# Optimization experiments

Hardware: AMD Instinct MI355X
Metric: run time of the kernel (lower is better)

Reference implementation:

```python
import jax, jax.numpy as jnp
import numpy as np

DECAY = 0.99
EPS = 1e-5
K = 512  # num_embeddings


def setup_inputs() -> dict:
    key = jax.random.key(0)
    k1, k2, k3 = jax.random.split(key, 3)
    B, C, H, W = 32, 64, 64, 64
    x = jax.random.normal(k1, (B, C, H, W), dtype=jnp.float32)
    codebook = jax.random.uniform(k2, (K, C), dtype=jnp.float32)
    ema_cluster_size = jnp.ones((K,), dtype=jnp.float32)
    ema_weight = jax.random.uniform(k3, (K, C), dtype=jnp.float32)
    return {"x": x, "codebook": codebook,
            "ema_cluster_size": ema_cluster_size, "ema_weight": ema_weight}


def reference(x, codebook, ema_cluster_size, ema_weight):
    B, C, H, W = x.shape
    # (B, C, H, W) -> (B*H*W, C)
    x_flat = jnp.transpose(x, (0, 2, 3, 1)).reshape(-1, C)

    x_sq = jnp.sum(x_flat * x_flat, axis=1, keepdims=True)        # [N, 1]
    e_sq = jnp.sum(codebook * codebook, axis=1)[None, :]          # [1, K]
    distances = x_sq + e_sq - 2.0 * (x_flat @ codebook.T)         # [N, K]
    indices = jnp.argmin(distances, axis=1)                        # [N]

    quantized = codebook[indices].reshape(B, H, W, C)
    quantized = jnp.transpose(quantized, (0, 3, 1, 2))             # [B, C, H, W]

    # EMA codebook update (training path); one-hot matmuls expressed as segment sums
    counts = jax.ops.segment_sum(jnp.ones_like(indices, dtype=x.dtype), indices,
                                 num_segments=K)                   # [K]
    sums = jax.ops.segment_sum(x_flat, indices, num_segments=K)    # [K, C]
    new_cluster_size = DECAY * ema_cluster_size + (1.0 - DECAY) * counts
    new_ema_weight = DECAY * ema_weight + (1.0 - DECAY) * sums
    n = jnp.sum(new_cluster_size)
    smoothed = (new_cluster_size + EPS) / (n + K * EPS) * n
    new_codebook = new_ema_weight / smoothed[:, None]

    commitment_loss = jnp.mean((x - jax.lax.stop_gradient(quantized)) ** 2)
    unique_codes = jnp.sum(counts > 0).astype(jnp.float32)

    out = x + jax.lax.stop_gradient(quantized - x)  # straight-through estimator
    return out, commitment_loss, unique_codes, new_codebook
```

## Files before the change

### kernel.cpp

```cpp
#include <hip/hip_runtime.h>


typedef __attribute__((ext_vector_type(8))) short bf16x8;
typedef __attribute__((ext_vector_type(16))) float f32x16;

#define MFMA32 __builtin_amdgcn_mfma_f32_32x32x16_bf16
#define NSEG 256

__device__ __forceinline__ unsigned short f2bf(float f) {
    unsigned u = __float_as_uint(f);
    return (unsigned short)((u + 0x7fffu + ((u >> 16) & 1u)) >> 16);
}
__device__ __forceinline__ float bf2f(unsigned short h) {
    return __uint_as_float(((unsigned)h) << 16);
}

__global__ void __launch_bounds__(512)
vq_prep(const float* __restrict__ cb, float* __restrict__ esq, char* __restrict__ cbF) {
    __shared__ float tile[64 * 65];
    const int tid = threadIdx.x;
    const int k0  = blockIdx.x * 64;
    #pragma unroll
    for (int i = tid; i < 4096; i += 512)
        tile[(i >> 6) * 65 + (i & 63)] = cb[k0 * 64 + i];
    __syncthreads();
    const int u  = tid >> 6;
    const int kl = tid & 63;
    const float* row = tile + kl * 65;
    const int cbase = (u >> 1) * 16 + (u & 1) * 8;
    bf16x8 h8, l8;
    #pragma unroll
    for (int j = 0; j < 8; ++j) {
        float e = row[cbase + j];
        unsigned short hb = f2bf(e);
        float lo = e - bf2f(hb);
        h8[j] = (short)hb;
        l8[j] = (short)f2bf(lo);
    }
    const size_t idx = (size_t)(u * 512 + k0 + kl) * 16;
    *(bf16x8*)(cbF + idx)         = h8;
    *(bf16x8*)(cbF + 65536 + idx) = l8;
    if (u == 0) {
        float s = 0.f;
        #pragma unroll
        for (int c = 0; c < 64; ++c) { float v = row[c]; s = fmaf(v, v, s); }
        esq[k0 + kl] = s;
    }
}

__device__ __forceinline__ void upd(float s, int kq, float& b1, int& q1, float& b2, int& q2) {
    bool t1 = s < b1;
    bool t2 = s < b2;
    float nb2 = t1 ? b1 : (t2 ? s : b2);
    int   nq2 = t1 ? q1 : (t2 ? kq : q2);
    b2 = nb2; q2 = nq2;
    b1 = t1 ? s : b1;
    q1 = t1 ? kq : q1;
}

__device__ __forceinline__ int refine_pair(int k1, int k2, long gx,
        const float* __restrict__ x, const float* __restrict__ cbg,
        const float* esq) {
    const float4* e1 = (const float4*)(cbg + (k1 << 6));
    const float4* e2 = (const float4*)(cbg + (k2 << 6));
    float a0 = 0.f, a1 = 0.f, c0 = 0.f, c1 = 0.f;
    #pragma unroll 4
    for (int j = 0; j < 16; ++j) {
        float4 ea = e1[j], eb = e2[j];
        float x0 = x[gx + (long)(4 * j + 0) * 4096];
        float x1 = x[gx + (long)(4 * j + 1) * 4096];
        float x2 = x[gx + (long)(4 * j + 2) * 4096];
        float x3 = x[gx + (long)(4 * j + 3) * 4096];
        a0 = fmaf(x0, ea.x, a0); a1 = fmaf(x1, ea.y, a1);
        a0 = fmaf(x2, ea.z, a0); a1 = fmaf(x3, ea.w, a1);
        c0 = fmaf(x0, eb.x, c0); c1 = fmaf(x1, eb.y, c1);
        c0 = fmaf(x2, eb.z, c0); c1 = fmaf(x3, eb.w, c1);
    }
    float s1 = esq[k1] - 2.f * (a0 + a1);
    float s2 = esq[k2] - 2.f * (c0 + c1);
    return (s2 < s1 || (s2 == s1 && k2 < k1)) ? k2 : k1;
}

#define AM_LDS_FLOATS 16896

__global__ void __launch_bounds__(512, 2)
vq_argmin(const float* __restrict__ x, const float* __restrict__ cbg,
          const float* __restrict__ esqg, const char* __restrict__ cbF,
          unsigned short* __restrict__ bkg, float* __restrict__ zero528) {
    extern __shared__ float lds[];
    float* esq = lds + 16384;
    const bf16x8* chi   = (const bf16x8*)lds;
    const bf16x8* clo_g = (const bf16x8*)(cbF + 65536);
    const int tid  = threadIdx.x;
    const int lane = tid & 63;
    const int wv   = tid >> 6;
    const int l31  = lane & 31;
    const int hh   = lane >> 5;

    {
        const float4* src = (const float4*)cbF;
        float4* dst = (float4*)lds;
        #pragma unroll
        for (int i = tid; i < 4096; i += 512) dst[i] = src[i];
        esq[tid] = esqg[tid];
    }
    zero528[tid] = 0.f;
    if (tid < 16) zero528[512 + tid] = 0.f;

    const int nb = blockIdx.x * 256 + wv * 32;
    bf16x8 Bh[4], Bl[4];
    {
        const int n = nb + l31;
        const long gx = (long)(n >> 12) * 262144 + (long)((n >> 6) & 63) * 64 + (n & 63);
        #pragma unroll
        for (int cs = 0; cs < 4; ++cs) {
            float v[8];
            #pragma unroll
            for (int j = 0; j < 8; ++j)
                v[j] = -2.f * x[gx + (long)(cs * 16 + hh * 8 + j) * 4096];
            union { unsigned u[4]; bf16x8 v8; } uh, ul;
            #pragma unroll
            for (int p = 0; p < 4; ++p) {
                unsigned hp, lp;
                asm("v_cvt_pk_bf16_f32 %0, %1, %2" : "=v"(hp) : "v"(v[2*p]), "v"(v[2*p+1]));
                float r0 = v[2*p]     - __uint_as_float(hp << 16);
                float r1 = v[2*p + 1] - __uint_as_float(hp & 0xFFFF0000u);
                asm("v_cvt_pk_bf16_f32 %0, %1, %2" : "=v"(lp) : "v"(r0), "v"(r1));
                uh.u[p] = hp; ul.u[p] = lp;
            }
            Bh[cs] = uh.v8; Bl[cs] = ul.v8;
        }
    }
    __syncthreads();

    float b1 = 3.4e38f, b2 = 3.4e38f;
    int   q1 = 0, q2 = 0;
    bf16x8 Xl[4], Yl[4];

#define LOADAL(Al, kt) { _Pragma("unroll") for (int cs = 0; cs < 4; ++cs) { \
        Al[cs] = clo_g[(cs * 2 + hh) * 512 + (kt) * 32 + l31]; } }

#define STEP(Al, kt) { \
        bf16x8 Ah[4]; \
        _Pragma("unroll") for (int cs = 0; cs < 4; ++cs) \
            Ah[cs] = chi[(cs * 2 + hh) * 512 + (kt) * 32 + l31]; \
        f32x16 acc; \
        _Pragma("unroll") for (int g = 0; g < 4; ++g) { \
            float4 e4 = *(const float4*)(esq + (kt) * 32 + 8 * g + 4 * hh); \
            acc[4*g] = e4.x; acc[4*g+1] = e4.y; acc[4*g+2] = e4.z; acc[4*g+3] = e4.w; } \
        _Pragma("unroll") for (int cs = 0; cs < 4; ++cs) { \
            acc = MFMA32(Ah[cs], Bh[cs], acc, 0, 0, 0); \
            acc = MFMA32(Al[cs], Bh[cs], acc, 0, 0, 0); \
            acc = MFMA32(Ah[cs], Bl[cs], acc, 0, 0, 0); } \
        _Pragma("unroll") for (int e = 0; e < 16; ++e) { \
            int kq = (kt) * 32 + (e & 3) + 8 * (e >> 2); \
            upd(acc[e], kq, b1, q1, b2, q2); } }

    LOADAL(Xl, 0)
    #pragma unroll 1
    for (int ktp = 0; ktp < 16; ktp += 2) {
        LOADAL(Yl, ktp + 1)
        STEP(Xl, ktp)
        if (ktp + 2 < 16) LOADAL(Xl, ktp + 2)
        STEP(Yl, ktp + 1)
    }

    {
        float mb1 = b1, mb2 = b2;
        int   mk1 = q1 + 4 * hh, mk2 = q2 + 4 * hh;
        float ob1 = __shfl_xor(mb1, 32, 64); int ok1 = __shfl_xor(mk1, 32, 64);
        float ob2 = __shfl_xor(mb2, 32, 64); int ok2 = __shfl_xor(mk2, 32, 64);
        bool t = (ob1 < mb1) || (ob1 == mb1 && ok1 < mk1);
        float w1 = t ? ob1 : mb1;  int wk1 = t ? ok1 : mk1;
        float l1 = t ? mb1 : ob1;  int lk1 = t ? mk1 : ok1;
        float w2c = t ? ob2 : mb2; int wk2c = t ? ok2 : mk2;
        bool t2 = (w2c < l1) || (w2c == l1 && wk2c < lk1);
        float w2 = t2 ? w2c : l1;  int wk2 = t2 ? wk2c : lk1;
        if (hh == 0) {
            int kk = wk1;
            if (wk2 != wk1 && (w2 - w1 < 2e-3f)) {
                const int n = nb + l31;
                const long gx = (long)(n >> 12) * 262144
                              + (long)((n >> 6) & 63) * 64 + (n & 63);
                kk = refine_pair(wk1, wk2, gx, x, cbg, esq);
            }
            bkg[nb + l31] = (unsigned short)kk;
        }
    }
#undef LOADAL
#undef STEP
}

#define FUSED_LDS_BYTES (33536 * 2)

__global__ void __launch_bounds__(512)
vq_fused(const float* __restrict__ x, const float* __restrict__ cbg,
         const unsigned short* __restrict__ bkg, float* __restrict__ out,
         float* __restrict__ hsum, float* __restrict__ acc_loss,
         float* __restrict__ slabs) {
    extern __shared__ unsigned short sm16[];
    const int tid = threadIdx.x;
    if (blockIdx.x < 256) {
        float* hist = (float*)sm16;
        float* lred = (float*)sm16 + 512;
        hist[tid] = 0.f;
        __syncthreads();
        const int n  = blockIdx.x * 512 + tid;
        const long gx = (long)(n >> 12) * 262144 + (long)((n >> 6) & 63) * 64 + (n & 63);
        const int k1 = bkg[n];
        atomicAdd(&hist[k1], 1.0f);
        const float4* q4 = (const float4*)(cbg + (k1 << 6));
        float lsum = 0.f;
        #pragma unroll
        for (int j = 0; j < 16; ++j) {
            float4 q = q4[j];
            const float qv[4] = {q.x, q.y, q.z, q.w};
            #pragma unroll
            for (int r = 0; r < 4; ++r) {
                const int c = 4 * j + r;
                float xc = x[gx + (long)c * 4096];
                out[gx + (long)c * 4096] = qv[r];
                float d = xc - qv[r];
                lsum = fmaf(d, d, lsum);
            }
        }
        #pragma unroll
        for (int o = 32; o > 0; o >>= 1) lsum += __shfl_down(lsum, o, 64);
        if ((tid & 63) == 0) lred[tid >> 6] = lsum;
        __syncthreads();
        if (tid == 0) {
            float l = ((lred[0] + lred[1]) + (lred[2] + lred[3]))
                    + ((lred[4] + lred[5]) + (lred[6] + lred[7]));
            atomicAdd(acc_loss, l);
        }
        { float v = hist[tid]; if (v != 0.f) atomicAdd(&hsum[tid], v); }
    } else {
        unsigned short* xb = sm16;
        unsigned short* kb = sm16 + 33024;
        const int lane = tid & 63;
        const int w    = tid >> 6;
        const int l31  = lane & 31;
        const int hh   = lane >> 5;
        const int bix  = blockIdx.x - 256;
        const int n0   = bix * 512;
        const float* xpl = x + (long)(n0 >> 12) * 262144 + (n0 & 4095);

        kb[tid] = bkg[n0 + tid];
        #pragma unroll
        for (int i = 0; i < 16; ++i) {
            const int f  = tid + i * 512;
            const int c  = f >> 7;
            const int n4 = (f & 127) << 2;
            float4 v = *(const float4*)(xpl + (long)c * 4096 + n4);
            ushort4 o;
            o.x = f2bf(v.x); o.y = f2bf(v.y); o.z = f2bf(v.z); o.w = f2bf(v.w);
            *(ushort4*)(xb + c * 516 + n4) = o;
        }
        __syncthreads();

        const int t0 = w * 32 + l31;
        const int t1 = (w + 8) * 32 + l31;
        f32x16 aA0 = {}, aA1 = {}, aB0 = {}, aB1 = {};

        #pragma unroll 1
        for (int b16 = 0; b16 < 32; ++b16) {
            const int nofs = b16 * 16 + hh * 8;
            ushort4 p0a = *(const ushort4*)(xb + l31 * 516 + nofs);
            ushort4 p0b = *(const ushort4*)(xb + l31 * 516 + nofs + 4);
            ushort4 p1a = *(const ushort4*)(xb + (32 + l31) * 516 + nofs);
            ushort4 p1b = *(const ushort4*)(xb + (32 + l31) * 516 + nofs + 4);
            bf16x8 Bf0, Bf1;
            Bf0[0] = (short)p0a.x; Bf0[1] = (short)p0a.y;
            Bf0[2] = (short)p0a.z; Bf0[3] = (short)p0a.w;
            Bf0[4] = (short)p0b.x; Bf0[5] = (short)p0b.y;
            Bf0[6] = (short)p0b.z; Bf0[7] = (short)p0b.w;
            Bf1[0] = (short)p1a.x; Bf1[1] = (short)p1a.y;
            Bf1[2] = (short)p1a.z; Bf1[3] = (short)p1a.w;
            Bf1[4] = (short)p1b.x; Bf1[5] = (short)p1b.y;
            Bf1[6] = (short)p1b.z; Bf1[7] = (short)p1b.w;
            ushort4 k4a = *(const ushort4*)(kb + nofs);
            ushort4 k4b = *(const ushort4*)(kb + nofs + 4);
            const int kk[8] = {k4a.x, k4a.y, k4a.z, k4a.w,
                               k4b.x, k4b.y, k4b.z, k4b.w};
            bf16x8 A0, A1;
            #pragma unroll
            for (int j = 0; j < 8; ++j) {
                A0[j] = (kk[j] == t0) ? (short)0x3F80 : (short)0;
                A1[j] = (kk[j] == t1) ? (short)0x3F80 : (short)0;
            }
            aA0 = MFMA32(A0, Bf0, aA0, 0, 0, 0);
            aA1 = MFMA32(A0, Bf1, aA1, 0, 0, 0);
            aB0 = MFMA32(A1, Bf0, aB0, 0, 0, 0);
            aB1 = MFMA32(A1, Bf1, aB1, 0, 0, 0);
        }
        float* slab = slabs + (long)bix * 32768;
        #pragma unroll
        for (int e = 0; e < 16; ++e) {
            const int row = (e & 3) + 8 * (e >> 2) + 4 * hh;
            slab[(w * 32 + row) * 64 + l31]            = aA0[e];
            slab[(w * 32 + row) * 64 + 32 + l31]       = aA1[e];
            slab[((w + 8) * 32 + row) * 64 + l31]      = aB0[e];
            slab[((w + 8) * 32 + row) * 64 + 32 + l31] = aB1[e];
        }
    }
}

__global__ void __launch_bounds__(512)
vq_final(const float* __restrict__ slabs, const float* __restrict__ hsum,
         const float* __restrict__ acc_loss, const float* __restrict__ ema_cs,
         const float* __restrict__ ema_w, float* __restrict__ out_scalars,
         float* __restrict__ out_cb) {
    __shared__ float sm[512];
    __shared__ float s_red[17];
    const int tid = threadIdx.x;
    float cnt = hsum[tid];
    float ncs = 0.99f * ema_cs[tid] + 0.01f * cnt;
    float v1 = ncs;
    float v2 = (cnt > 0.f) ? 1.f : 0.f;
    #pragma unroll
    for (int o = 32; o > 0; o >>= 1) {
        v1 += __shfl_down(v1, o, 64);
        v2 += __shfl_down(v2, o, 64);
    }
    const int wv = tid >> 6;
    if ((tid & 63) == 0) { s_red[wv] = v1; s_red[wv + 8] = v2; }
    __syncthreads();
    if (tid == 0) {
        float nn = 0.f, uq = 0.f;
        #pragma unroll
        for (int i = 0; i < 8; ++i) { nn += s_red[i]; uq += s_red[i + 8]; }
        s_red[16] = nn;
        if (blockIdx.x == 0) {
            out_scalars[0] = acc_loss[0] / 8388608.f;
            out_scalars[1] = uq;
        }
    }
    __syncthreads();
    float nn = s_red[16];
    sm[tid] = (ncs + 1e-5f) / (nn + 512.f * 1e-5f) * nn;
    __syncthreads();
    const int e = blockIdx.x * 512 + tid;
    float s = 0.f;
    #pragma unroll 8
    for (int b = 0; b < NSEG; ++b) s += slabs[(long)b * 32768 + e];
    float nw = 0.99f * ema_w[e] + 0.01f * s;
    out_cb[e] = nw / sm[e >> 6];
}

extern "C" void kernel_launch(void* const* d_in, const int* in_sizes, int n_in,
                              void* d_out, int out_size, void* d_ws, size_t ws_size,
                              hipStream_t stream) {
    const float* x      = (const float*)d_in[0];
    const float* cb     = (const float*)d_in[1];
    const float* ema_cs = (const float*)d_in[2];
    const float* ema_w  = (const float*)d_in[3];

    float* out     = (float*)d_out;
    float* scalars = out + 8388608;
    float* out_cb  = out + 8388610;
    float* ws      = (float*)d_ws;

    float* slabs    = ws;
    float* hsum     = slabs + (size_t)NSEG * 32768;
    float* acc_loss = hsum + 512;
    float* esq      = acc_loss + 16;
    char*  cbF      = (char*)(esq + 512);
    unsigned short* bkg = (unsigned short*)(cbF + 131072);

    vq_prep<<<8, 512, 0, stream>>>(cb, esq, cbF);
    vq_argmin<<<512, 512, AM_LDS_FLOATS * sizeof(float), stream>>>(x, cb, esq, cbF, bkg, hsum);
    vq_fused<<<512, 512, FUSED_LDS_BYTES, stream>>>(x, cb, bkg, out, hsum, acc_loss, slabs);
    vq_final<<<64, 512, 0, stream>>>(slabs, hsum, acc_loss, ema_cs, ema_w, scalars, out_cb);
}
```

Before: 89.37 us.

## Fuse output gather, loss and histogram into argmin kernel epilogue

Moves the quantized-output write, commitment-loss accumulation and per-code histogram from the fused kernel into the end of the argmin kernel, reading indices from LDS instead of global memory. The segment-sum MFMA path becomes its own 256-block kernel. Zeroing of the histogram and loss accumulators moves into the prep kernel. This removes one pass that re-read x and the indices, but makes the argmin kernel longer and uses more LDS, which could cut its occupancy.

New measurement: 93.43 us. +4.5%, slower.

```diff
diff --git a/kernel.cpp b/kernel.cpp
--- a/kernel.cpp
+++ b/kernel.cpp
@@ -16,10 +16,13 @@
 }
 
 __global__ void __launch_bounds__(512)
-vq_prep(const float* __restrict__ cb, float* __restrict__ esq, char* __restrict__ cbF) {
+vq_prep(const float* __restrict__ cb, float* __restrict__ esq, char* __restrict__ cbF,
+        float* __restrict__ zero528) {
     __shared__ float tile[64 * 65];
     const int tid = threadIdx.x;
     const int k0  = blockIdx.x * 64;
+    zero528[tid] = 0.f;
+    if (tid < 16) zero528[512 + tid] = 0.f;
     #pragma unroll
     for (int i = tid; i < 4096; i += 512)
         tile[(i >> 6) * 65 + (i & 63)] = cb[k0 * 64 + i];
@@ -81,14 +84,18 @@
     return (s2 < s1 || (s2 == s1 && k2 < k1)) ? k2 : k1;
 }
 
-#define AM_LDS_FLOATS 16896
+#define AM_LDS_FLOATS 17672
 
 __global__ void __launch_bounds__(512, 2)
 vq_argmin(const float* __restrict__ x, const float* __restrict__ cbg,
           const float* __restrict__ esqg, const char* __restrict__ cbF,
-          unsigned short* __restrict__ bkg, float* __restrict__ zero528) {
+          unsigned short* __restrict__ bkg, float* __restrict__ hsum,
+          float* __restrict__ acc_loss, float* __restrict__ out) {
     extern __shared__ float lds[];
-    float* esq = lds + 16384;
+    float* esq  = lds + 16384;
+    int*   bki  = (int*)(lds + 16896);
+    float* hist = lds + 17152;
+    float* lred = lds + 17664;
     const bf16x8* chi   = (const bf16x8*)lds;
     const bf16x8* clo_g = (const bf16x8*)(cbF + 65536);
     const int tid  = threadIdx.x;
@@ -103,9 +110,8 @@
         #pragma unroll
         for (int i = tid; i < 4096; i += 512) dst[i] = src[i];
         esq[tid] = esqg[tid];
-    }
-    zero528[tid] = 0.f;
-    if (tid < 16) zero528[512 + tid] = 0.f;
+        hist[tid] = 0.f;
+    }
 
     const int nb = blockIdx.x * 256 + wv * 32;
     bf16x8 Bh[4], Bl[4];
@@ -185,39 +191,27 @@
                 kk = refine_pair(wk1, wk2, gx, x, cbg, esq);
             }
             bkg[nb + l31] = (unsigned short)kk;
-        }
-    }
-#undef LOADAL
-#undef STEP
-}
-
-#define FUSED_LDS_BYTES (33536 * 2)
-
-__global__ void __launch_bounds__(512)
-vq_fused(const float* __restrict__ x, const float* __restrict__ cbg,
-         const unsigned short* __restrict__ bkg, float* __restrict__ out,
-         float* __restrict__ hsum, float* __restrict__ acc_loss,
-         float* __restrict__ slabs) {
-    extern __shared__ unsigned short sm16[];
-    const int tid = threadIdx.x;
-    if (blockIdx.x < 256) {
-        float* hist = (float*)sm16;
-        float* lred = (float*)sm16 + 512;
-        hist[tid] = 0.f;
-        __syncthreads();
-        const int n  = blockIdx.x * 512 + tid;
+            bki[wv * 32 + l31] = kk;
+        }
+    }
+    __syncthreads();
+
+    {
+        const int nl = tid >> 1;
+        const int ch = (tid & 1) << 5;
+        const int n  = blockIdx.x * 256 + nl;
         const long gx = (long)(n >> 12) * 262144 + (long)((n >> 6) & 63) * 64 + (n & 63);
-        const int k1 = bkg[n];
-        atomicAdd(&hist[k1], 1.0f);
-        const float4* q4 = (const float4*)(cbg + (k1 << 6));
+        const int k1 = bki[nl];
+        if ((tid & 1) == 0) atomicAdd(&hist[k1], 1.0f);
+        const float4* q4 = (const float4*)(cbg + (k1 << 6) + ch);
         float lsum = 0.f;
         #pragma unroll
-        for (int j = 0; j < 16; ++j) {
+        for (int j = 0; j < 8; ++j) {
             float4 q = q4[j];
             const float qv[4] = {q.x, q.y, q.z, q.w};
             #pragma unroll
             for (int r = 0; r < 4; ++r) {
-                const int c = 4 * j + r;
+                const int c = ch + 4 * j + r;
                 float xc = x[gx + (long)c * 4096];
                 out[gx + (long)c * 4096] = qv[r];
                 float d = xc - qv[r];
@@ -226,82 +220,92 @@
         }
         #pragma unroll
         for (int o = 32; o > 0; o >>= 1) lsum += __shfl_down(lsum, o, 64);
-        if ((tid & 63) == 0) lred[tid >> 6] = lsum;
-        __syncthreads();
-        if (tid == 0) {
-            float l = ((lred[0] + lred[1]) + (lred[2] + lred[3]))
-                    + ((lred[4] + lred[5]) + (lred[6] + lred[7]));
-            atomicAdd(acc_loss, l);
-        }
-        { float v = hist[tid]; if (v != 0.f) atomicAdd(&hsum[tid], v); }
-    } else {
-        unsigned short* xb = sm16;
-        unsigned short* kb = sm16 + 33024;
-        const int lane = tid & 63;
-        const int w    = tid >> 6;
-        const int l31  = lane & 31;
-        const int hh   = lane >> 5;
-        const int bix  = blockIdx.x - 256;
-        const int n0   = bix * 512;
-        const float* xpl = x + (long)(n0 >> 12) * 262144 + (n0 & 4095);
-
-        kb[tid] = bkg[n0 + tid];
-        #pragma unroll
-        for (int i = 0; i < 16; ++i) {
-            const int f  = tid + i * 512;
-            const int c  = f >> 7;
-            const int n4 = (f & 127) << 2;
-            float4 v = *(const float4*)(xpl + (long)c * 4096 + n4);
-            ushort4 o;
-            o.x = f2bf(v.x); o.y = f2bf(v.y); o.z = f2bf(v.z); o.w = f2bf(v.w);
-            *(ushort4*)(xb + c * 516 + n4) = o;
-        }
-        __syncthreads();
-
-        const int t0 = w * 32 + l31;
-        const int t1 = (w + 8) * 32 + l31;
-        f32x16 aA0 = {}, aA1 = {}, aB0 = {}, aB1 = {};
-
-        #pragma unroll 1
-        for (int b16 = 0; b16 < 32; ++b16) {
-            const int nofs = b16 * 16 + hh * 8;
-            ushort4 p0a = *(const ushort4*)(xb + l31 * 516 + nofs);
-            ushort4 p0b = *(const ushort4*)(xb + l31 * 516 + nofs + 4);
-            ushort4 p1a = *(const ushort4*)(xb + (32 + l31) * 516 + nofs);
-            ushort4 p1b = *(const ushort4*)(xb + (32 + l31) * 516 + nofs + 4);
-            bf16x8 Bf0, Bf1;
-            Bf0[0] = (short)p0a.x; Bf0[1] = (short)p0a.y;
-            Bf0[2] = (short)p0a.z; Bf0[3] = (short)p0a.w;
-            Bf0[4] = (short)p0b.x; Bf0[5] = (short)p0b.y;
-            Bf0[6] = (short)p0b.z; Bf0[7] = (short)p0b.w;
-            Bf1[0] = (short)p1a.x; Bf1[1] = (short)p1a.y;
-            Bf1[2] = (short)p1a.z; Bf1[3] = (short)p1a.w;
-            Bf1[4] = (short)p1b.x; Bf1[5] = (short)p1b.y;
-            Bf1[6] = (short)p1b.z; Bf1[7] = (short)p1b.w;
-            ushort4 k4a = *(const ushort4*)(kb + nofs);
-            ushort4 k4b = *(const ushort4*)(kb + nofs + 4);
-            const int kk[8] = {k4a.x, k4a.y, k4a.z, k4a.w,
-                               k4b.x, k4b.y, k4b.z, k4b.w};
-            bf16x8 A0, A1;
-            #pragma unroll
-            for (int j = 0; j < 8; ++j) {
-                A0[j] = (kk[j] == t0) ? (short)0x3F80 : (short)0;
-                A1[j] = (kk[j] == t1) ? (short)0x3F80 : (short)0;
-            }
-            aA0 = MFMA32(A0, Bf0, aA0, 0, 0, 0);
-            aA1 = MFMA32(A0, Bf1, aA1, 0, 0, 0);
-            aB0 = MFMA32(A1, Bf0, aB0, 0, 0, 0);
-            aB1 = MFMA32(A1, Bf1, aB1, 0, 0, 0);
-        }
-        float* slab = slabs + (long)bix * 32768;
-        #pragma unroll
-        for (int e = 0; e < 16; ++e) {
-            const int row = (e & 3) + 8 * (e >> 2) + 4 * hh;
-            slab[(w * 32 + row) * 64 + l31]            = aA0[e];
-            slab[(w * 32 + row) * 64 + 32 + l31]       = aA1[e];
-            slab[((w + 8) * 32 + row) * 64 + l31]      = aB0[e];
-            slab[((w + 8) * 32 + row) * 64 + 32 + l31] = aB1[e];
-        }
+        if (lane == 0) lred[wv] = lsum;
+    }
+    __syncthreads();
+    if (tid == 0) {
+        float l = ((lred[0] + lred[1]) + (lred[2] + lred[3]))
+                + ((lred[4] + lred[5]) + (lred[6] + lred[7]));
+        atomicAdd(acc_loss, l);
+    }
+    { float v = hist[tid]; if (v != 0.f) atomicAdd(&hsum[tid], v); }
+#undef LOADAL
+#undef STEP
+}
+
+#define SEG_LDS_BYTES (33536 * 2)
+
+__global__ void __launch_bounds__(512)
+vq_segsum(const float* __restrict__ x, const unsigned short* __restrict__ bkg,
+          float* __restrict__ slabs) {
+    extern __shared__ unsigned short sm16[];
+    unsigned short* xb = sm16;
+    unsigned short* kb = sm16 + 33024;
+    const int tid  = threadIdx.x;
+    const int lane = tid & 63;
+    const int w    = tid >> 6;
+    const int l31  = lane & 31;
+    const int hh   = lane >> 5;
+    const int bix  = blockIdx.x;
+    const int n0   = bix * 512;
+    const float* xpl = x + (long)(n0 >> 12) * 262144 + (n0 & 4095);
+
+    kb[tid] = bkg[n0 + tid];
+    #pragma unroll
+    for (int i = 0; i < 16; ++i) {
+        const int f  = tid + i * 512;
+        const int c  = f >> 7;
+        const int n4 = (f & 127) << 2;
+        float4 v = *(const float4*)(xpl + (long)c * 4096 + n4);
+        ushort4 o;
+        o.x = f2bf(v.x); o.y = f2bf(v.y); o.z = f2bf(v.z); o.w = f2bf(v.w);
+        *(ushort4*)(xb + c * 516 + n4) = o;
+    }
+    __syncthreads();
+
+    const int t0 = w * 32 + l31;
+    const int t1 = (w + 8) * 32 + l31;
+    f32x16 aA0 = {}, aA1 = {}, aB0 = {}, aB1 = {};
+
+    #pragma unroll 1
+    for (int b16 = 0; b16 < 32; ++b16) {
+        const int nofs = b16 * 16 + hh * 8;
+        ushort4 p0a = *(const ushort4*)(xb + l31 * 516 + nofs);
+        ushort4 p0b = *(const ushort4*)(xb + l31 * 516 + nofs + 4);
+        ushort4 p1a = *(const ushort4*)(xb + (32 + l31) * 516 + nofs);
+        ushort4 p1b = *(const ushort4*)(xb + (32 + l31) * 516 + nofs + 4);
+        bf16x8 Bf0, Bf1;
+        Bf0[0] = (short)p0a.x; Bf0[1] = (short)p0a.y;
+        Bf0[2] = (short)p0a.z; Bf0[3] = (short)p0a.w;
+        Bf0[4] = (short)p0b.x; Bf0[5] = (short)p0b.y;
+        Bf0[6] = (short)p0b.z; Bf0[7] = (short)p0b.w;
+        Bf1[0] = (short)p1a.x; Bf1[1] = (short)p1a.y;
+        Bf1[2] = (short)p1a.z; Bf1[3] = (short)p1a.w;
+        Bf1[4] = (short)p1b.x; Bf1[5] = (short)p1b.y;
+        Bf1[6] = (short)p1b.z; Bf1[7] = (short)p1b.w;
+        ushort4 k4a = *(const ushort4*)(kb + nofs);
+        ushort4 k4b = *(const ushort4*)(kb + nofs + 4);
+        const int kk[8] = {k4a.x, k4a.y, k4a.z, k4a.w,
+                           k4b.x, k4b.y, k4b.z, k4b.w};
+        bf16x8 A0, A1;
+        #pragma unroll
+        for (int j = 0; j < 8; ++j) {
+            A0[j] = (kk[j] == t0) ? (short)0x3F80 : (short)0;
+            A1[j] = (kk[j] == t1) ? (short)0x3F80 : (short)0;
+        }
+        aA0 = MFMA32(A0, Bf0, aA0, 0, 0, 0);
+        aA1 = MFMA32(A0, Bf1, aA1, 0, 0, 0);
+        aB0 = MFMA32(A1, Bf0, aB0, 0, 0, 0);
+        aB1 = MFMA32(A1, Bf1, aB1, 0, 0, 0);
+    }
+    float* slab = slabs + (long)bix * 32768;
+    #pragma unroll
+    for (int e = 0; e < 16; ++e) {
+        const int row = (e & 3) + 8 * (e >> 2) + 4 * hh;
+        slab[(w * 32 + row) * 64 + l31]            = aA0[e];
+        slab[(w * 32 + row) * 64 + 32 + l31]       = aA1[e];
+        slab[((w + 8) * 32 + row) * 64 + l31]      = aB0[e];
+        slab[((w + 8) * 32 + row) * 64 + 32 + l31] = aB1[e];
     }
 }
 
@@ -367,8 +371,9 @@
     char*  cbF      = (char*)(esq + 512);
     unsigned short* bkg = (unsigned short*)(cbF + 131072);
 
-    vq_prep<<<8, 512, 0, stream>>>(cb, esq, cbF);
-    vq_argmin<<<512, 512, AM_LDS_FLOATS * sizeof(float), stream>>>(x, cb, esq, cbF, bkg, hsum);
-    vq_fused<<<512, 512, FUSED_LDS_BYTES, stream>>>(x, cb, bkg, out, hsum, acc_loss, slabs);
+    vq_prep<<<8, 512, 0, stream>>>(cb, esq, cbF, hsum);
+    vq_argmin<<<512, 512, AM_LDS_FLOATS * sizeof(float), stream>>>(
+        x, cb, esq, cbF, bkg, hsum, acc_loss, out);
+    vq_segsum<<<256, 512, SEG_LDS_BYTES, stream>>>(x, bkg, slabs);
     vq_final<<<64, 512, 0, stream>>>(slabs, hsum, acc_loss, ema_cs, ema_w, scalars, out_cb);
 }
```
